# Kernel optimization log

Measured on AMD Instinct MI355X. Metric: run time of the kernel, lower is better.

The kernel has to match this reference:

```python
import jax, jax.numpy as jnp
import numpy as np

MAX_NORM = 10.0
NUM_LAYERS = 3
MARGIN = 0.1
VAE_BETA = 0.1
EPS = 1e-7
N_NODES = 100000


def logmap0(x):
    # Lorentz (k=1) log map at origin: first coord -> 0, spatial scaled
    x0 = x[..., :1]
    alpha = jnp.maximum(x0, 1.0 + EPS)
    coef = jnp.arccosh(alpha) / jnp.sqrt(jnp.maximum(alpha * alpha - 1.0, EPS))
    return jnp.concatenate([jnp.zeros_like(x0), coef * x[..., 1:]], axis=-1)


def expmap0(u, project=False):
    # Lorentz (k=1) exp map at origin; first coord of u is ignored (tangent at o)
    sp = u[..., 1:]
    n = jnp.maximum(jnp.linalg.norm(sp, axis=-1, keepdims=True), EPS)
    x_sp = jnp.sinh(n) / n * sp
    if project:
        sn = jnp.linalg.norm(x_sp, axis=-1, keepdims=True)
        x_sp = x_sp * jnp.minimum(1.0, MAX_NORM / jnp.maximum(sn, EPS))
        x0 = jnp.sqrt(1.0 + jnp.sum(x_sp * x_sp, axis=-1, keepdims=True))
    else:
        x0 = jnp.cosh(n)
    return jnp.concatenate([x0, x_sp], axis=-1)


def sqdist(x, y):
    inner = -x[..., 0] * y[..., 0] + jnp.sum(x[..., 1:] * y[..., 1:], axis=-1)
    d = jnp.arccosh(jnp.maximum(-inner, 1.0 + EPS))
    return d * d


def moe(x, W, b, gW, gb):
    gates = jax.nn.softmax(x @ gW + gb, axis=-1)              # [N,E]
    expert = jnp.einsum('nd,edo->neo', x, W) + b               # [N,E,D]
    return jnp.einsum('neo,ne->no', expert, gates)             # [N,D]


def spmm(rows, cols, vals, h):
    return jax.ops.segment_sum(vals[:, None] * h[cols], rows, num_segments=N_NODES)


def setup_inputs() -> dict:
    key = jax.random.key(0)
    ks = jax.random.split(key, 24)
    D, E, NNZ, T = 64, 8, 3200000, 262144
    Nu, Ni = 60000, 40000
    s = 0.05
    emb_user = expmap0(jax.random.normal(ks[0], (Nu, D)) * 0.1, project=True)
    emb_item = expmap0(jax.random.normal(ks[1], (Ni, D)) * 0.1, project=True)
    return {
        'emb_user': emb_user,
        'emb_item': emb_item,
        'adj_rows': jax.random.randint(ks[2], (NNZ,), 0, N_NODES, dtype=jnp.int32),
        'adj_cols': jax.random.randint(ks[3], (NNZ,), 0, N_NODES, dtype=jnp.int32),
        'adj_vals': jax.random.uniform(ks[4], (NNZ,)) * 0.05,
        'triples': jax.random.randint(ks[5], (T, 3), 0, N_NODES, dtype=jnp.int32),
        'eps': jax.random.normal(ks[6], (N_NODES, D)),
        'tW': jax.random.normal(ks[7], (E, D, D)) * s,
        'tb': jax.random.normal(ks[8], (E, D)) * s,
        'tgW': jax.random.normal(ks[9], (D, E)) * s,
        'tgb': jax.random.normal(ks[10], (E,)) * s,
        'muW': jax.random.normal(ks[11], (D, D)) * s,
        'mub': jax.random.normal(ks[12], (D,)) * s,
        'lvW': jax.random.normal(ks[13], (D, D)) * s,
        'lvb': jax.random.normal(ks[14], (D,)) * s,
        'f1W': jax.random.normal(ks[15], (D, 2 * D)) * s,
        'f1b': jax.random.normal(ks[16], (2 * D,)) * s,
        'f2W': jax.random.normal(ks[17], (2 * D, D)) * s,
        'f2b': jax.random.normal(ks[18], (D,)) * s,
        'dW': jax.random.normal(ks[19], (E, D, D)) * s,
        'db': jax.random.normal(ks[20], (E, D)) * s,
        'dgW': jax.random.normal(ks[21], (D, E)) * s,
        'dgb': jax.random.normal(ks[22], (E,)) * s,
    }


def reference(emb_user, emb_item, adj_rows, adj_cols, adj_vals, triples, eps,
              tW, tb, tgW, tgb, muW, mub, lvW, lvb,
              f1W, f1b, f2W, f2b, dW, db, dgW, dgb):
    # encode: log map frozen hyperbolic embeddings, MoE transform
    t = jnp.concatenate([logmap0(emb_user), logmap0(emb_item)], axis=0)   # [N,D]
    m = moe(t, tW, tb, tgW, tgb)                                          # [N,D]
    # VAE
    mu = m @ muW + mub
    logvar = m @ lvW + lvb
    std = jnp.exp(0.5 * logvar)
    z = expmap0(mu + eps * std, project=True)
    # hyperbolic decoder
    h = logmap0(z)
    h = jax.nn.relu(h @ f1W + f1b)
    h = h @ f2W + f2b
    h = moe(h, dW, db, dgW, dgb)
    recon = expmap0(h, project=True)
    recon_loss = jnp.mean(sqdist(recon, expmap0(m)))
    kl_loss = -0.5 * jnp.mean(1.0 + logvar - mu * mu - jnp.exp(logvar))
    # margin loss: num_layers of sparse propagation, sum of layer outputs
    res = m
    out_sum = jnp.zeros_like(m)
    for _ in range(NUM_LAYERS):
        res = spmm(adj_rows, adj_cols, adj_vals, res)
        out_sum = out_sum + res
    out = expmap0(out_sum, project=True)
    a, p, n = out[triples[:, 0]], out[triples[:, 1]], out[triples[:, 2]]
    margin_loss = jnp.sum(jax.nn.relu(sqdist(a, p) - sqdist(a, n) + MARGIN))
    return margin_loss + VAE_BETA * (recon_loss + kl_loss)
```

## Files before the change

### kernel.cpp

```cpp
#include <hip/hip_runtime.h>
#include <math.h>

#define EPSF 1e-7f
#define MAXNRM 10.0f
#define NB 782
#define RPB 128
#define EPT 16

using bf16x8 = __attribute__((ext_vector_type(8))) short;
using f32x4  = __attribute__((ext_vector_type(4))) float;
typedef unsigned short u16;

__device__ __forceinline__ float wsum(float v) {
    #pragma unroll
    for (int off = 32; off > 0; off >>= 1) v += __shfl_xor(v, off, 64);
    return v;
}

__device__ __forceinline__ u16 f2bf(float x) {
    unsigned u = __float_as_uint(x);
    unsigned r = (u + 0x7FFFu + ((u >> 16) & 1u)) >> 16;
    return (u16)r;
}
__device__ __forceinline__ float bflo(unsigned u) { return __uint_as_float(u << 16); }
__device__ __forceinline__ float bfhi(unsigned u) { return __uint_as_float(u & 0xFFFF0000u); }


__device__ __forceinline__ void body_logmap(int bid, const float* __restrict__ eu,
                                            const float* __restrict__ ei, int Nu, int Ntot,
                                            float* __restrict__ out) {
    const int lane = threadIdx.x & 63;
    const int g = lane >> 4, q = lane & 15;
    const int n = bid * 16 + (threadIdx.x >> 6) * 4 + g;
    if (n >= Ntot) return;
    const float* src = (n < Nu) ? (eu + (size_t)n * 64) : (ei + (size_t)(n - Nu) * 64);
    const float x0 = src[0];
    const float alpha = fmaxf(x0, 1.0f + EPSF);
    const float coef = acoshf(alpha) / sqrtf(fmaxf(alpha * alpha - 1.0f, EPSF));
    const float4 v = *(const float4*)(src + q * 4);
    float4 o;
    o.x = (q == 0) ? 0.0f : coef * v.x;
    o.y = coef * v.y; o.z = coef * v.z; o.w = coef * v.w;
    *(float4*)(out + ((size_t)n << 6) + q * 4) = o;
}

__device__ __forceinline__ void body_bhist(int bid, int nblk, const int* __restrict__ rows,
                                           int nnz, int* __restrict__ bhist, int* h) {
    for (int j = threadIdx.x; j < NB; j += 256) h[j] = 0;
    __syncthreads();
    for (int i = bid * 256 + threadIdx.x; i < nnz; i += nblk * 256)
        atomicAdd(&h[rows[i] >> 7], 1);
    __syncthreads();
    for (int j = threadIdx.x; j < NB; j += 256)
        if (h[j]) atomicAdd(&bhist[j], h[j]);
}

__device__ __forceinline__ void body_moe(int bid, char* smem,
    const float* __restrict__ X, float* __restrict__ Y,
    const u16* __restrict__ Wt, const u16* __restrict__ Bt,
    const float* __restrict__ GW, const float* __restrict__ GB,
    u16* __restrict__ Bhout, int Ntot)
{
    float (*sX)[68] = (float(*)[68])smem;
    float (*sG)[8]  = (float(*)[8])(smem + 17408);
    float* sGW      = (float*)(smem + 17408 + 2048);
    const int tid = threadIdx.x;
    const int n0 = bid * 64;

    for (int i = tid; i < 64 * 16; i += 256) {
        const int rr = i >> 4, cc = i & 15;
        float4 v = make_float4(0.f, 0.f, 0.f, 0.f);
        if (n0 + rr < Ntot) v = *(const float4*)(X + (size_t)(n0 + rr) * 64 + cc * 4);
        *(float4*)&sX[rr][cc * 4] = v;
    }
    for (int i = tid; i < 512; i += 256) sGW[i] = GW[i];
    __syncthreads();

    {
        const int n = tid >> 2, e0 = (tid & 3) * 2;
        float lg0 = GB[e0], lg1 = GB[e0 + 1];
        #pragma unroll 8
        for (int d = 0; d < 64; ++d) {
            const float xv = sX[n][d];
            lg0 += xv * sGW[d * 8 + e0];
            lg1 += xv * sGW[d * 8 + e0 + 1];
        }
        sG[n][e0] = lg0; sG[n][e0 + 1] = lg1;
    }
    __syncthreads();
    if (tid < 64) {
        float ex[8], mx = -1e30f, s = 0.f;
        #pragma unroll
        for (int e = 0; e < 8; ++e) mx = fmaxf(mx, sG[tid][e]);
        #pragma unroll
        for (int e = 0; e < 8; ++e) { ex[e] = expf(sG[tid][e] - mx); s += ex[e]; }
        const float inv = 1.0f / s;
        #pragma unroll
        for (int e = 0; e < 8; ++e) sG[tid][e] = ex[e] * inv;
    }
    __syncthreads();

    const int w = tid >> 6, l = tid & 63;
    const int m = l & 15, kq = l >> 4;
    const int col = w * 16 + m;

    f32x4 zero = {0.f, 0.f, 0.f, 0.f};
    f32x4 acc[4];
    #pragma unroll
    for (int rt = 0; rt < 4; ++rt) acc[rt] = zero;

    bf16x8 bcur = *(const bf16x8*)(Wt + (((size_t)col) << 6) + kq * 8);

    #pragma unroll
    for (int kk = 0; kk < 16; ++kk) {
        const int e = kk >> 1;
        const int d0 = (kk & 1) * 32 + kq * 8;
        bf16x8 bnext = bcur;
        if (kk < 15) {
            const int e2 = (kk + 1) >> 1;
            const int d02 = ((kk + 1) & 1) * 32 + kq * 8;
            bnext = *(const bf16x8*)(Wt + (((size_t)(e2 * 64 + col)) << 6) + d02);
        }
        #pragma unroll
        for (int rt = 0; rt < 4; ++rt) {
            const int row = rt * 16 + m;
            const float gme = sG[row][e];
            const float4 xa = *(const float4*)&sX[row][d0];
            const float4 xb = *(const float4*)&sX[row][d0 + 4];
            union { bf16x8 v; u16 u[8]; } af;
            af.u[0] = f2bf(gme * xa.x); af.u[1] = f2bf(gme * xa.y);
            af.u[2] = f2bf(gme * xa.z); af.u[3] = f2bf(gme * xa.w);
            af.u[4] = f2bf(gme * xb.x); af.u[5] = f2bf(gme * xb.y);
            af.u[6] = f2bf(gme * xb.z); af.u[7] = f2bf(gme * xb.w);
            acc[rt] = __builtin_amdgcn_mfma_f32_16x16x32_bf16(af.v, bcur, acc[rt], 0, 0, 0);
        }
        bcur = bnext;
    }
    {
        bf16x8 z8 = {0, 0, 0, 0, 0, 0, 0, 0};
        bf16x8 bb = z8;
        if (kq == 0) bb = *(const bf16x8*)(Bt + (col << 3));
        #pragma unroll
        for (int rt = 0; rt < 4; ++rt) {
            union { bf16x8 v; u16 u[8]; } af;
            #pragma unroll
            for (int j = 0; j < 8; ++j)
                af.u[j] = (kq == 0) ? f2bf(sG[rt * 16 + m][j]) : (u16)0;
            acc[rt] = __builtin_amdgcn_mfma_f32_16x16x32_bf16(af.v, bb, acc[rt], 0, 0, 0);
        }
    }

    #pragma unroll
    for (int rt = 0; rt < 4; ++rt) {
        #pragma unroll
        for (int r = 0; r < 4; ++r) {
            const int row = rt * 16 + kq * 4 + r;
            if (n0 + row < Ntot) {
                Y[(size_t)(n0 + row) * 64 + col] = acc[rt][r];
                if (Bhout)
                    Bhout[(((size_t)(n0 + row)) << 6) + col] = f2bf(acc[rt][r]);
            }
        }
    }
}

__device__ __forceinline__ void body_bscatter(int bid, char* smem,
    const int* __restrict__ rows, const int* __restrict__ cols,
    const float* __restrict__ vals, int nnz,
    int* __restrict__ gcur, int2* __restrict__ tmp)
{
    int* lh = (int*)smem;
    int* lb = (int*)(smem + 3128);
    const int tid = threadIdx.x;
    for (int j = tid; j < NB; j += 256) lh[j] = 0;
    __syncthreads();

    const int base = bid * (256 * EPT);
    int r[EPT], c[EPT], lp[EPT];
    float v[EPT];
    #pragma unroll
    for (int j = 0; j < EPT; ++j) {
        const int i = base + j * 256 + tid;
        if (i < nnz) {
            r[j] = rows[i]; c[j] = cols[i]; v[j] = vals[i];
            lp[j] = atomicAdd(&lh[r[j] >> 7], 1);
        }
    }
    __syncthreads();
    for (int j = tid; j < NB; j += 256)
        if (lh[j]) lb[j] = atomicAdd(&gcur[j], lh[j]);
    __syncthreads();
    #pragma unroll
    for (int j = 0; j < EPT; ++j) {
        const int i = base + j * 256 + tid;
        if (i < nnz) {
            int2 e;
            e.x = ((r[j] & 127) << 17) | c[j];
            e.y = __float_as_int(v[j]);
            tmp[lb[r[j] >> 7] + lp[j]] = e;
        }
    }
}

__device__ __forceinline__ void body_vae(int bid, char* smem,
    const float* __restrict__ M, float* __restrict__ Hout,
    const float* __restrict__ EPSN, const u16* __restrict__ WtV,
    const float* __restrict__ mub, const float* __restrict__ lvb,
    float* __restrict__ klslot, int Ntot)
{
    float (*sX)[68] = (float(*)[68])smem;
    float* sC       = (float*)(smem + 17408);
    const int tid = threadIdx.x;
    const int n0 = bid * 64;

    for (int i = tid; i < 64 * 16; i += 256) {
        const int rr = i >> 4, cc = i & 15;
        float4 v = make_float4(0.f, 0.f, 0.f, 0.f);
        if (n0 + rr < Ntot) v = *(const float4*)(M + (size_t)(n0 + rr) * 64 + cc * 4);
        *(float4*)&sX[rr][cc * 4] = v;
    }
    __syncthreads();

    const int w = tid >> 6, l = tid & 63;
    const int m = l & 15, kq = l >> 4;
    const int rowm = w * 16 + m;

    f32x4 zero = {0.f, 0.f, 0.f, 0.f};
    f32x4 acc[8];
    #pragma unroll
    for (int t = 0; t < 8; ++t) acc[t] = zero;

    #pragma unroll
    for (int ks = 0; ks < 2; ++ks) {
        const int k0 = ks * 32 + kq * 8;
        const float4 xa = *(const float4*)&sX[rowm][k0];
        const float4 xb = *(const float4*)&sX[rowm][k0 + 4];
        union { bf16x8 v; u16 u[8]; } af;
        af.u[0] = f2bf(xa.x); af.u[1] = f2bf(xa.y); af.u[2] = f2bf(xa.z); af.u[3] = f2bf(xa.w);
        af.u[4] = f2bf(xb.x); af.u[5] = f2bf(xb.y); af.u[6] = f2bf(xb.z); af.u[7] = f2bf(xb.w);
        #pragma unroll
        for (int t = 0; t < 8; ++t) {
            const bf16x8 bf = *(const bf16x8*)(WtV + (((size_t)(t * 16 + m)) << 6) + k0);
            acc[t] = __builtin_amdgcn_mfma_f32_16x16x32_bf16(af.v, bf, acc[t], 0, 0, 0);
        }
    }

    float klp = 0.f;
    float uv[4][4];
    #pragma unroll
    for (int t = 0; t < 4; ++t) {
        const int col = t * 16 + m;
        const float mb = mub[col], lb = lvb[col];
        #pragma unroll
        for (int r = 0; r < 4; ++r) {
            const int row = w * 16 + kq * 4 + r;
            const float mu = acc[t][r] + mb;
            const float lv = acc[t + 4][r] + lb;
            const float elv = expf(lv);
            float ep = 0.f;
            if (n0 + row < Ntot) {
                klp += 1.0f + lv - mu * mu - elv;
                ep = EPSN[(size_t)(n0 + row) * 64 + col];
            }
            uv[t][r] = mu + ep * expf(0.5f * lv);
        }
    }
    klp = wsum(klp);
    if (l == 0) atomicAdd(&klslot[(bid * 4 + w) & 255], klp);

    #pragma unroll
    for (int t = 0; t < 4; ++t)
        #pragma unroll
        for (int r = 0; r < 4; ++r)
            sX[w * 16 + kq * 4 + r][t * 16 + m] = uv[t][r];
    __syncthreads();

    {
        const int r2 = tid >> 2, j = tid & 3;
        float ss = 0.f;
        #pragma unroll
        for (int jj = 0; jj < 4; ++jj) {
            float4 a = *(const float4*)&sX[r2][j * 16 + jj * 4];
            if (j == 0 && jj == 0) a.x = 0.f;
            ss += a.x * a.x + a.y * a.y + a.z * a.z + a.w * a.w;
        }
        ss += __shfl_xor(ss, 1, 64);
        ss += __shfl_xor(ss, 2, 64);
        if (j == 0) {
            const float nr = fmaxf(sqrtf(ss), EPSF);
            const float r = sinhf(nr) / nr;
            const float sn = r * sqrtf(ss);
            const float scale = fminf(1.0f, MAXNRM / fmaxf(sn, EPSF));
            const float mult = r * scale;
            const float s2 = mult * mult * ss;
            const float z0 = sqrtf(1.0f + s2);
            const float alpha = fmaxf(z0, 1.0f + EPSF);
            const float coef = acoshf(alpha) / sqrtf(fmaxf(alpha * alpha - 1.0f, EPSF));
            sC[r2] = coef * mult;
        }
    }
    __syncthreads();

    for (int i = tid; i < 64 * 16; i += 256) {
        const int rr = i >> 4, cc = i & 15;
        if (n0 + rr >= Ntot) continue;
        const float4 v = *(const float4*)&sX[rr][cc * 4];
        const float sc = sC[rr];
        float4 o;
        o.x = (cc == 0) ? 0.f : sc * v.x;
        o.y = sc * v.y; o.z = sc * v.z; o.w = sc * v.w;
        *(float4*)(Hout + (size_t)(n0 + rr) * 64 + cc * 4) = o;
    }
}

__device__ __forceinline__ void body_sort(int bid, char* smem,
    const int2* __restrict__ tmp, const int* __restrict__ bstart,
    int2* __restrict__ sedge, int* __restrict__ Fout, int Ntot, int nnz)
{
    int* cnt  = (int*)smem;
    int* excl = (int*)(smem + 512);
    const int b = bid;
    const int tid = threadIdx.x;
    if (tid < RPB) cnt[tid] = 0;
    __syncthreads();
    const int s = bstart[b], t = bstart[b + 1];

    for (int i = s + tid; i < t; i += 256)
        atomicAdd(&cnt[((unsigned)tmp[i].x) >> 17], 1);
    __syncthreads();

    if (tid < 64) {
        const int a0 = cnt[2 * tid], a1 = cnt[2 * tid + 1];
        const int pairsum = a0 + a1;
        int run = pairsum;
        #pragma unroll
        for (int off = 1; off < 64; off <<= 1) {
            const int vv = __shfl_up(run, off, 64);
            if (tid >= off) run += vv;
        }
        const int ep = run - pairsum;
        excl[2 * tid] = ep;
        excl[2 * tid + 1] = ep + a0;
    }
    __syncthreads();

    const int r0 = b << 7;
    if (tid < RPB) {
        const int r = r0 + tid;
        if (r < Ntot) Fout[r] = s + excl[tid];
        cnt[tid] = excl[tid];
    }
    if (b == NB - 1 && tid == 0) Fout[Ntot] = nnz;
    __syncthreads();

    for (int i = s + tid; i < t; i += 256) {
        const int2 e = tmp[i];
        const int rib = ((unsigned)e.x) >> 17;
        const int lpos = atomicAdd(&cnt[rib], 1);
        int2 o; o.x = e.x & 0x1FFFF; o.y = e.y;
        sedge[s + lpos] = o;
    }
}


__global__ __launch_bounds__(256) void fat_prep(
    const float* tW, const float* tb, u16* Wt1, u16* Bt1,
    const float* dW, const float* db, u16* Wt2, u16* Bt2,
    const float* muW, const float* lvW, u16* WtV,
    const float* f1W, u16* Wt1f, const float* f2W, u16* Wt2f)
{
    const int b = blockIdx.x;
    if (b < 36) {
        const float* W = (b < 18) ? tW : dW;
        const float* Bb = (b < 18) ? tb : db;
        u16* Wt = (b < 18) ? Wt1 : Wt2;
        u16* Bt = (b < 18) ? Bt1 : Bt2;
        const int i = (b % 18) * 256 + threadIdx.x;
        if (i < 4096) {
            const int e = i >> 9, o = (i >> 3) & 63, dbi = i & 7;
            u16 v[8];
            #pragma unroll
            for (int j = 0; j < 8; ++j)
                v[j] = f2bf(W[((size_t)e << 12) + (size_t)(dbi * 8 + j) * 64 + o]);
            uint4 p;
            p.x = (unsigned)v[0] | ((unsigned)v[1] << 16);
            p.y = (unsigned)v[2] | ((unsigned)v[3] << 16);
            p.z = (unsigned)v[4] | ((unsigned)v[5] << 16);
            p.w = (unsigned)v[6] | ((unsigned)v[7] << 16);
            *(uint4*)(Wt + (((size_t)(e * 64 + o)) << 6) + dbi * 8) = p;
        } else if (i < 4096 + 512) {
            const int j = i - 4096, o = j >> 3, e = j & 7;
            Bt[o * 8 + e] = f2bf(Bb[e * 64 + o]);
        }
    } else if (b < 68) {
        const bool is_mu = (b < 52);
        const float* src = is_mu ? muW : lvW;
        u16* dst = is_mu ? WtV : (WtV + 4096);
        const int i = ((b - (is_mu ? 36 : 52))) * 256 + threadIdx.x;
        if (i < 4096) {
            const int o = i / 64, k = i - o * 64;
            dst[i] = f2bf(src[k * 64 + o]);
        }
    } else if (b < 100) {
        const int i = (b - 68) * 256 + threadIdx.x;
        if (i < 8192) {
            const int o = i / 64, k = i - o * 64;
            Wt1f[i] = f2bf(f1W[k * 128 + o]);
        }
    } else {
        const int i = (b - 100) * 256 + threadIdx.x;
        if (i < 8192) {
            const int o = i / 128, k = i - o * 128;
            Wt2f[i] = f2bf(f2W[k * 64 + o]);
        }
    }
}

#define NB_LOG 6250
#define NB_HIST 512
__global__ __launch_bounds__(256) void fat_log_bhist(
    const float* eu, const float* ei, int Nu, int Ntot, float* out,
    const int* rows, int nnz, int* bhist)
{
    __shared__ int h[NB];
    const int b = blockIdx.x;
    if (b < NB_LOG) {
        body_logmap(b, eu, ei, Nu, Ntot, out);
    } else {
        body_bhist(b - NB_LOG, NB_HIST, rows, nnz, bhist, h);
    }
}

#define NB_MOE 1563
__global__ __launch_bounds__(256) void fat_moe_bsc(
    const float* X, float* Y, const u16* Wt, const u16* Bt,
    const float* GW, const float* GB, u16* Bhout, int Ntot,
    const int* rows, const int* cols, const float* vals, int nnz,
    int* gcur, int2* tmp)
{
    __shared__ __align__(16) char smem[21504];
    const int b = blockIdx.x;
    if (b < NB_MOE) {
        body_moe(b, smem, X, Y, Wt, Bt, GW, GB, Bhout, Ntot);
    } else {
        body_bscatter(b - NB_MOE, smem, rows, cols, vals, nnz, gcur, tmp);
    }
}

__global__ __launch_bounds__(256) void fat_vae_sort(
    const float* M, float* Hout, const float* EPSN, const u16* WtV,
    const float* mub, const float* lvb, float* klslot, int Ntot,
    const int2* tmp, const int* bstart, int2* sedge, int* Fout, int nnz)
{
    __shared__ __align__(16) char smem[17664];
    const int b = blockIdx.x;
    if (b < NB_MOE) {
        body_vae(b, smem, M, Hout, EPSN, WtV, mub, lvb, klslot, Ntot);
    } else {
        body_sort(b - NB_MOE, smem, tmp, bstart, sedge, Fout, Ntot, nnz);
    }
}


__global__ __launch_bounds__(256) void k_moe_mfma(
    const float* __restrict__ X, float* __restrict__ Y,
    const u16* __restrict__ Wt, const u16* __restrict__ Bt,
    const float* __restrict__ GW, const float* __restrict__ GB,
    u16* __restrict__ Bhout, int Ntot)
{
    __shared__ __align__(16) char smem[21504];
    body_moe(blockIdx.x, smem, X, Y, Wt, Bt, GW, GB, Bhout, Ntot);
}

__global__ __launch_bounds__(1024) void k_bscan(const int* __restrict__ bhist,
                                                int* __restrict__ bstart, int* __restrict__ gcur) {
    __shared__ int s[1024];
    const int tid = threadIdx.x;
    int v = (tid < NB) ? bhist[tid] : 0;
    s[tid] = v;
    __syncthreads();
    for (int off = 1; off < 1024; off <<= 1) {
        int t = (tid >= off) ? s[tid - off] : 0;
        __syncthreads();
        s[tid] += t;
        __syncthreads();
    }
    if (tid < NB) {
        bstart[tid + 1] = s[tid];
        gcur[tid] = s[tid] - v;
        if (tid == 0) bstart[0] = 0;
    }
}

__global__ __launch_bounds__(256) void k_ffn_mfma(
    float* __restrict__ Hio,
    const u16* __restrict__ Wt1f, const float* __restrict__ f1b,
    const u16* __restrict__ Wt2f, const float* __restrict__ f2b, int Ntot)
{
    __shared__ float sH[64][68];
    __shared__ u16 sH1[64][136];
    const int tid = threadIdx.x;
    const int n0 = blockIdx.x * 64;

    for (int i = tid; i < 64 * 16; i += 256) {
        const int rr = i >> 4, cc = i & 15;
        float4 v = make_float4(0.f, 0.f, 0.f, 0.f);
        if (n0 + rr < Ntot) v = *(const float4*)(Hio + (size_t)(n0 + rr) * 64 + cc * 4);
        *(float4*)&sH[rr][cc * 4] = v;
    }
    __syncthreads();

    const int w = tid >> 6, l = tid & 63;
    const int m = l & 15, kq = l >> 4;
    const int rowm = w * 16 + m;

    f32x4 zero = {0.f, 0.f, 0.f, 0.f};
    f32x4 acc1[8];
    #pragma unroll
    for (int t = 0; t < 8; ++t) acc1[t] = zero;

    #pragma unroll
    for (int ks = 0; ks < 2; ++ks) {
        const int k0 = ks * 32 + kq * 8;
        const float4 xa = *(const float4*)&sH[rowm][k0];
        const float4 xb = *(const float4*)&sH[rowm][k0 + 4];
        union { bf16x8 v; u16 u[8]; } af;
        af.u[0] = f2bf(xa.x); af.u[1] = f2bf(xa.y); af.u[2] = f2bf(xa.z); af.u[3] = f2bf(xa.w);
        af.u[4] = f2bf(xb.x); af.u[5] = f2bf(xb.y); af.u[6] = f2bf(xb.z); af.u[7] = f2bf(xb.w);
        #pragma unroll
        for (int t = 0; t < 8; ++t) {
            const bf16x8 bf = *(const bf16x8*)(Wt1f + (((size_t)(t * 16 + m)) << 6) + k0);
            acc1[t] = __builtin_amdgcn_mfma_f32_16x16x32_bf16(af.v, bf, acc1[t], 0, 0, 0);
        }
    }
    #pragma unroll
    for (int t = 0; t < 8; ++t) {
        const float bb = f1b[t * 16 + m];
        #pragma unroll
        for (int r = 0; r < 4; ++r)
            sH1[w * 16 + kq * 4 + r][t * 16 + m] = f2bf(fmaxf(acc1[t][r] + bb, 0.f));
    }
    __syncthreads();

    f32x4 acc2[4];
    #pragma unroll
    for (int t = 0; t < 4; ++t) acc2[t] = zero;
    #pragma unroll
    for (int ks = 0; ks < 4; ++ks) {
        const int k0 = ks * 32 + kq * 8;
        const bf16x8 af = *(const bf16x8*)&sH1[rowm][k0];
        #pragma unroll
        for (int t = 0; t < 4; ++t) {
            const bf16x8 bf = *(const bf16x8*)(Wt2f + (((size_t)(t * 16 + m)) << 7) + k0);
            acc2[t] = __builtin_amdgcn_mfma_f32_16x16x32_bf16(af, bf, acc2[t], 0, 0, 0);
        }
    }
    #pragma unroll
    for (int t = 0; t < 4; ++t) {
        const float bb = f2b[t * 16 + m];
        #pragma unroll
        for (int r = 0; r < 4; ++r) {
            const int row = w * 16 + kq * 4 + r;
            if (n0 + row < Ntot)
                Hio[(size_t)(n0 + row) * 64 + t * 16 + m] = acc2[t][r] + bb;
        }
    }
}

__global__ __launch_bounds__(256) void k_recon(
    const float* __restrict__ HM, const float* __restrict__ M,
    int Ntot, float* __restrict__ slot)
{
    const int lane = threadIdx.x & 63;
    const int g = lane >> 4, q = lane & 15;
    const int n = blockIdx.x * 16 + (threadIdx.x >> 6) * 4 + g;

    float ssh = 0.f, ssm = 0.f, dot = 0.f;
    if (n < Ntot) {
        const float4 h = *(const float4*)(HM + ((size_t)n << 6) + q * 4);
        const float4 m = *(const float4*)(M  + ((size_t)n << 6) + q * 4);
        const float hx = (q == 0) ? 0.f : h.x;
        const float mx = (q == 0) ? 0.f : m.x;
        ssh = hx * hx + h.y * h.y + h.z * h.z + h.w * h.w;
        ssm = mx * mx + m.y * m.y + m.z * m.z + m.w * m.w;
        dot = hx * mx + h.y * m.y + h.z * m.z + h.w * m.w;
    }
    #pragma unroll
    for (int off = 1; off < 16; off <<= 1) {
        ssh += __shfl_xor(ssh, off, 64);
        ssm += __shfl_xor(ssm, off, 64);
        dot += __shfl_xor(dot, off, 64);
    }

    float part = 0.f;
    if (q == 0 && n < Ntot) {
        const float nm = fmaxf(sqrtf(ssm), EPSF);
        const float em0 = coshf(nm);
        const float rm = sinhf(nm) / nm;

        const float nh = fmaxf(sqrtf(ssh), EPSF);
        const float rh = sinhf(nh) / nh;
        const float sn = rh * sqrtf(ssh);
        const float scale = fminf(1.0f, MAXNRM / fmaxf(sn, EPSF));
        const float mult = rh * scale;
        const float rec0 = sqrtf(1.0f + mult * mult * ssh);

        const float inner = mult * rm * dot - rec0 * em0;
        const float dd = acoshf(fmaxf(-inner, 1.0f + EPSF));
        part = dd * dd;
    }
    part = wsum(part);
    __shared__ float sb[4];
    if (lane == 0) sb[threadIdx.x >> 6] = part;
    __syncthreads();
    if (threadIdx.x == 0)
        atomicAdd(&slot[blockIdx.x & 255], sb[0] + sb[1] + sb[2] + sb[3]);
}

__global__ __launch_bounds__(256) void k_spmm(
    const u16* __restrict__ in, u16* __restrict__ outb,
    const int* __restrict__ F, const int2* __restrict__ sedge, int Ntot, int nnz)
{
    const int r = blockIdx.x * 4 + (threadIdx.x >> 6);
    if (r >= Ntot) return;
    const int lane = threadIdx.x & 63;
    const int g = lane >> 3, q = lane & 7;
    const int e0 = F[r], e1 = F[r + 1];
    const int nnzm1 = nnz - 1;

    float acc0[8], acc1[8];
    #pragma unroll
    for (int j = 0; j < 8; ++j) { acc0[j] = 0.f; acc1[j] = 0.f; }

    int2 edA, edB;
    uint4 hbA, hbB;
    {
        const int ea = e0 + g, eb = e0 + 8 + g;
        edA = sedge[min(ea, nnzm1)]; if (ea >= e1) edA.y = 0;
        edB = sedge[min(eb, nnzm1)]; if (eb >= e1) edB.y = 0;
        hbA = *(const uint4*)(in + (((size_t)edA.x) << 6) + q * 8);
        hbB = *(const uint4*)(in + (((size_t)edB.x) << 6) + q * 8);
    }

    for (int base = e0; base < e1; base += 16) {
        const int na = base + 16 + g, nb = base + 24 + g;
        int2 edA2 = sedge[min(na, nnzm1)]; if (na >= e1) edA2.y = 0;
        int2 edB2 = sedge[min(nb, nnzm1)]; if (nb >= e1) edB2.y = 0;
        const uint4 hbA2 = *(const uint4*)(in + (((size_t)edA2.x) << 6) + q * 8);
        const uint4 hbB2 = *(const uint4*)(in + (((size_t)edB2.x) << 6) + q * 8);

        {
            const float v = __int_as_float(edA.y);
            acc0[0] += v * bflo(hbA.x);
            acc0[1] += v * bfhi(hbA.x);
            acc0[2] += v * bflo(hbA.y);
            acc0[3] += v * bfhi(hbA.y);
            acc0[4] += v * bflo(hbA.z);
            acc0[5] += v * bfhi(hbA.z);
            acc0[6] += v * bflo(hbA.w);
            acc0[7] += v * bfhi(hbA.w);
        }
        {
            const float v = __int_as_float(edB.y);
            acc1[0] += v * bflo(hbB.x);
            acc1[1] += v * bfhi(hbB.x);
            acc1[2] += v * bflo(hbB.y);
            acc1[3] += v * bfhi(hbB.y);
            acc1[4] += v * bflo(hbB.z);
            acc1[5] += v * bfhi(hbB.z);
            acc1[6] += v * bflo(hbB.w);
            acc1[7] += v * bfhi(hbB.w);
        }
        edA = edA2; edB = edB2; hbA = hbA2; hbB = hbB2;
    }
    float a0[8];
    #pragma unroll
    for (int j = 0; j < 8; ++j) a0[j] = acc0[j] + acc1[j];

    #pragma unroll
    for (int off = 8; off < 64; off <<= 1)
        #pragma unroll
        for (int j = 0; j < 8; ++j) a0[j] += __shfl_xor(a0[j], off, 64);

    if (g == 0) {
        const size_t ob = (((size_t)r) << 6) + q * 8;
        uint4 p;
        p.x = (unsigned)f2bf(a0[0]) | ((unsigned)f2bf(a0[1]) << 16);
        p.y = (unsigned)f2bf(a0[2]) | ((unsigned)f2bf(a0[3]) << 16);
        p.z = (unsigned)f2bf(a0[4]) | ((unsigned)f2bf(a0[5]) << 16);
        p.w = (unsigned)f2bf(a0[6]) | ((unsigned)f2bf(a0[7]) << 16);
        *(uint4*)(outb + ob) = p;
    }
}

__global__ __launch_bounds__(256) void k_osum(
    const u16* __restrict__ r1, const u16* __restrict__ r2,
    const u16* __restrict__ r3, u16* __restrict__ outb, int Ntot)
{
    const int lane = threadIdx.x & 63;
    const int g = lane >> 4, q = lane & 15;
    const int n = blockIdx.x * 16 + (threadIdx.x >> 6) * 4 + g;
    if (n >= Ntot) return;
    const size_t ob = ((size_t)n << 6) + q * 4;
    const uint2 a = *(const uint2*)(r1 + ob);
    const uint2 b = *(const uint2*)(r2 + ob);
    const uint2 c = *(const uint2*)(r3 + ob);
    float s0 = bflo(a.x) + bflo(b.x) + bflo(c.x);
    float s1 = bfhi(a.x) + bfhi(b.x) + bfhi(c.x);
    float s2 = bflo(a.y) + bflo(b.y) + bflo(c.y);
    float s3 = bfhi(a.y) + bfhi(b.y) + bfhi(c.y);
    const float v0 = (q == 0) ? 0.f : s0;
    float ss = v0 * v0 + s1 * s1 + s2 * s2 + s3 * s3;
    #pragma unroll
    for (int off = 1; off < 16; off <<= 1) ss += __shfl_xor(ss, off, 64);
    const float nr = fmaxf(sqrtf(ss), EPSF);
    const float r = sinhf(nr) / nr;
    const float sn = r * sqrtf(ss);
    const float scale = fminf(1.0f, MAXNRM / fmaxf(sn, EPSF));
    const float mult = r * scale;
    const float o0 = (q == 0) ? sqrtf(1.0f + mult * mult * ss) : mult * s0;
    uint2 p;
    p.x = (unsigned)f2bf(o0) | ((unsigned)f2bf(mult * s1) << 16);
    p.y = (unsigned)f2bf(mult * s2) | ((unsigned)f2bf(mult * s3) << 16);
    *(uint2*)(outb + ob) = p;
}

__global__ __launch_bounds__(256) void k_triples(
    const u16* __restrict__ Ob, const int* __restrict__ tri,
    int T, float* __restrict__ slot)
{
    const int lane = threadIdx.x & 63;
    const int g = lane >> 4, q = lane & 15;
    const int wid = blockIdx.x * 4 + (threadIdx.x >> 6);
    const int stride = gridDim.x * 4 * 4;

    float racc = 0.f;
    int t = wid * 4 + g;

    uint2 ca, cp, cn;
    if (t < T) {
        const int a = tri[3 * t], p = tri[3 * t + 1], nn = tri[3 * t + 2];
        ca = *(const uint2*)(Ob + (((size_t)a) << 6) + q * 4);
        cp = *(const uint2*)(Ob + (((size_t)p) << 6) + q * 4);
        cn = *(const uint2*)(Ob + (((size_t)nn) << 6) + q * 4);
    }

    for (; t < T; ) {
        const int tn = t + stride;
        const int tc = min(tn, T - 1);
        const int a2 = tri[3 * tc], p2 = tri[3 * tc + 1], n2 = tri[3 * tc + 2];
        const uint2 na_ = *(const uint2*)(Ob + (((size_t)a2) << 6) + q * 4);
        const uint2 np_ = *(const uint2*)(Ob + (((size_t)p2) << 6) + q * 4);
        const uint2 nn_ = *(const uint2*)(Ob + (((size_t)n2) << 6) + q * 4);

        {
            const float a0 = bflo(ca.x), a1 = bfhi(ca.x), a2f = bflo(ca.y), a3 = bfhi(ca.y);
            const float p0 = bflo(cp.x), p1 = bfhi(cp.x), p2f = bflo(cp.y), p3 = bfhi(cp.y);
            const float n0 = bflo(cn.x), n1 = bfhi(cn.x), n2f = bflo(cn.y), n3 = bfhi(cn.y);
            const float s0 = (q == 0) ? -1.f : 1.f;
            float i1 = s0 * a0 * p0 + a1 * p1 + a2f * p2f + a3 * p3;
            float i2 = s0 * a0 * n0 + a1 * n1 + a2f * n2f + a3 * n3;
            #pragma unroll
            for (int off = 1; off < 16; off <<= 1) {
                i1 += __shfl_xor(i1, off, 64);
                i2 += __shfl_xor(i2, off, 64);
            }
            if (q == 0) {
                const float d1 = acoshf(fmaxf(-i1, 1.0f + EPSF));
                const float d2 = acoshf(fmaxf(-i2, 1.0f + EPSF));
                const float l = d1 * d1 - d2 * d2 + 0.1f;
                if (l > 0.f) racc += l;
            }
        }
        ca = na_; cp = np_; cn = nn_;
        t = tn;
    }

    racc = wsum(racc);
    __shared__ float sb[4];
    if (lane == 0) sb[threadIdx.x >> 6] = racc;
    __syncthreads();
    if (threadIdx.x == 0)
        atomicAdd(&slot[blockIdx.x & 255], sb[0] + sb[1] + sb[2] + sb[3]);
}

__global__ void k_final(const float* __restrict__ slots, float* __restrict__ out, int Ntot)
{
    const int tid = threadIdx.x;
    float m = slots[tid], r = slots[256 + tid], k = slots[512 + tid];
    m = wsum(m); r = wsum(r); k = wsum(k);
    __shared__ float sm[4], sr[4], sk[4];
    if ((tid & 63) == 0) { sm[tid >> 6] = m; sr[tid >> 6] = r; sk[tid >> 6] = k; }
    __syncthreads();
    if (tid == 0) {
        const float M = sm[0] + sm[1] + sm[2] + sm[3];
        const float R = sr[0] + sr[1] + sr[2] + sr[3];
        const float K = sk[0] + sk[1] + sk[2] + sk[3];
        const float recon = R / (float)Ntot;
        const float kl = -0.5f * K / ((float)Ntot * 64.0f);
        out[0] = M + 0.1f * (recon + kl);
    }
}

extern "C" void kernel_launch(void* const* d_in, const int* in_sizes, int n_in,
                              void* d_out, int out_size, void* d_ws, size_t ws_size,
                              hipStream_t stream)
{
    const float* emb_user = (const float*)d_in[0];
    const float* emb_item = (const float*)d_in[1];
    const int*   adj_rows = (const int*)d_in[2];
    const int*   adj_cols = (const int*)d_in[3];
    const float* adj_vals = (const float*)d_in[4];
    const int*   triples  = (const int*)d_in[5];
    const float* epsin    = (const float*)d_in[6];
    const float* tW  = (const float*)d_in[7];
    const float* tb  = (const float*)d_in[8];
    const float* tgW = (const float*)d_in[9];
    const float* tgb = (const float*)d_in[10];
    const float* muW = (const float*)d_in[11];
    const float* mub = (const float*)d_in[12];
    const float* lvW = (const float*)d_in[13];
    const float* lvb = (const float*)d_in[14];
    const float* f1W = (const float*)d_in[15];
    const float* f1b = (const float*)d_in[16];
    const float* f2W = (const float*)d_in[17];
    const float* f2b = (const float*)d_in[18];
    const float* dW  = (const float*)d_in[19];
    const float* db  = (const float*)d_in[20];
    const float* dgW = (const float*)d_in[21];
    const float* dgb = (const float*)d_in[22];

    const int Nu = in_sizes[0] / 64, Ni = in_sizes[1] / 64;
    const int N = Nu + Ni;
    const int NNZ = in_sizes[4];
    const int T = in_sizes[5] / 3;

    float* ws = (float*)d_ws;
    size_t off = 0;
    float* slots = ws + off; off += 1024;
    float* A  = ws + off; off += (size_t)N * 64;
    float* B  = ws + off; off += (size_t)N * 64;
    float* C  = ws + off; off += (size_t)N * 64;
    float* D  = ws + off; off += (size_t)N * 64;
    float* E  = ws + off; off += (size_t)N * 64;
    int*   F  = (int*)(ws + off); off += (size_t)N + 64;
    int*   bstart = (int*)(ws + off); off += 1024;
    int*   bhist  = (int*)(ws + off); off += 1024;
    int*   gcur   = (int*)(ws + off); off += 1024;
    u16* Wt1 = (u16*)(ws + off); off += 16384;
    u16* Bt1 = (u16*)(ws + off); off += 256;
    u16* Wt2 = (u16*)(ws + off); off += 16384;
    u16* Bt2 = (u16*)(ws + off); off += 256;
    u16* WtV  = (u16*)(ws + off); off += 4096;
    u16* Wt1f = (u16*)(ws + off); off += 4096;
    u16* Wt2f = (u16*)(ws + off); off += 4096;

    int2* tmp   = (int2*)C;
    int2* sedge = (int2*)D;
    u16* Bh  = (u16*)E;
    u16* Hb1 = (u16*)E + (size_t)N * 64;
    u16* Hb2 = (u16*)C;
    u16* Hb3 = (u16*)A;
    u16* Ob  = (u16*)B;

    hipMemsetAsync(slots, 0, 1024 * sizeof(float), stream);
    hipMemsetAsync(bhist, 0, 1024 * sizeof(int), stream);

    const int nb16 = (N + 15) / 16;
    const int nb64 = (N + 63) / 64;
    const int ns1 = (NNZ + 256 * EPT - 1) / (256 * EPT);

    fat_prep<<<132, 256, 0, stream>>>(tW, tb, Wt1, Bt1, dW, db, Wt2, Bt2,
                                      muW, lvW, WtV, f1W, Wt1f, f2W, Wt2f);

    fat_log_bhist<<<NB_LOG + NB_HIST, 256, 0, stream>>>(emb_user, emb_item, Nu, N, A,
                                                        adj_rows, NNZ, bhist);

    k_bscan<<<1, 1024, 0, stream>>>(bhist, bstart, gcur);

    fat_moe_bsc<<<NB_MOE + 782, 256, 0, stream>>>(A, B, Wt1, Bt1, tgW, tgb, Bh, N,
                                                  adj_rows, adj_cols, adj_vals, NNZ, gcur, tmp);

    fat_vae_sort<<<NB_MOE + NB, 256, 0, stream>>>(B, A, epsin, WtV, mub, lvb, slots + 512, N,
                                                  tmp, bstart, sedge, F, NNZ);

    k_ffn_mfma<<<nb64, 256, 0, stream>>>(A, Wt1f, f1b, Wt2f, f2b, N);
    k_moe_mfma<<<nb64, 256, 0, stream>>>(A, C, Wt2, Bt2, dgW, dgb, nullptr, N);
    k_recon<<<nb16, 256, 0, stream>>>(C, B, N, slots + 256);

    k_spmm<<<(N + 3) / 4, 256, 0, stream>>>(Bh,  Hb1, F, sedge, N, NNZ);
    k_spmm<<<(N + 3) / 4, 256, 0, stream>>>(Hb1, Hb2, F, sedge, N, NNZ);
    k_spmm<<<(N + 3) / 4, 256, 0, stream>>>(Hb2, Hb3, F, sedge, N, NNZ);

    k_osum<<<nb16, 256, 0, stream>>>(Hb1, Hb2, Hb3, Ob, N);

    k_triples<<<2048, 256, 0, stream>>>(Ob, triples, T, slots);
    k_final<<<1, 256, 0, stream>>>(slots, (float*)d_out, N);
}
```

Baseline: 459.7 us.

## Co-schedule decoder FFN, MoE and recon blocks with the three SpMM passes

Merges the decoder stages (FFN, second MoE, recon loss) with the three independent sparse propagation passes into three combined kernels, dispatching blocks by index to either the dense body or the SpMM body. The aim is to run compute-bound MFMA work alongside the memory-bound gathers and to remove separate launches. The second SpMM output now reuses the buffer that held the first SpMM's input, because C is written concurrently by the MoE. In exchange, SpMM blocks now carry the larger shared-memory allocation of the combined kernels, which may reduce their occupancy.

```diff
diff --git a/kernel.cpp b/kernel.cpp
--- a/kernel.cpp
+++ b/kernel.cpp
@@ -359,6 +359,208 @@
         const int lpos = atomicAdd(&cnt[rib], 1);
         int2 o; o.x = e.x & 0x1FFFF; o.y = e.y;
         sedge[s + lpos] = o;
+    }
+}
+
+__device__ __forceinline__ void body_ffn(int bid, char* smem,
+    float* __restrict__ Hio,
+    const u16* __restrict__ Wt1f, const float* __restrict__ f1b,
+    const u16* __restrict__ Wt2f, const float* __restrict__ f2b, int Ntot)
+{
+    float (*sH)[68] = (float(*)[68])smem;
+    u16 (*sH1)[136] = (u16(*)[136])smem;
+    const int tid = threadIdx.x;
+    const int n0 = bid * 64;
+
+    for (int i = tid; i < 64 * 16; i += 256) {
+        const int rr = i >> 4, cc = i & 15;
+        float4 v = make_float4(0.f, 0.f, 0.f, 0.f);
+        if (n0 + rr < Ntot) v = *(const float4*)(Hio + (size_t)(n0 + rr) * 64 + cc * 4);
+        *(float4*)&sH[rr][cc * 4] = v;
+    }
+    __syncthreads();
+
+    const int w = tid >> 6, l = tid & 63;
+    const int m = l & 15, kq = l >> 4;
+    const int rowm = w * 16 + m;
+
+    f32x4 zero = {0.f, 0.f, 0.f, 0.f};
+    f32x4 acc1[8];
+    #pragma unroll
+    for (int t = 0; t < 8; ++t) acc1[t] = zero;
+
+    #pragma unroll
+    for (int ks = 0; ks < 2; ++ks) {
+        const int k0 = ks * 32 + kq * 8;
+        const float4 xa = *(const float4*)&sH[rowm][k0];
+        const float4 xb = *(const float4*)&sH[rowm][k0 + 4];
+        union { bf16x8 v; u16 u[8]; } af;
+        af.u[0] = f2bf(xa.x); af.u[1] = f2bf(xa.y); af.u[2] = f2bf(xa.z); af.u[3] = f2bf(xa.w);
+        af.u[4] = f2bf(xb.x); af.u[5] = f2bf(xb.y); af.u[6] = f2bf(xb.z); af.u[7] = f2bf(xb.w);
+        #pragma unroll
+        for (int t = 0; t < 8; ++t) {
+            const bf16x8 bf = *(const bf16x8*)(Wt1f + (((size_t)(t * 16 + m)) << 6) + k0);
+            acc1[t] = __builtin_amdgcn_mfma_f32_16x16x32_bf16(af.v, bf, acc1[t], 0, 0, 0);
+        }
+    }
+    __syncthreads();
+    #pragma unroll
+    for (int t = 0; t < 8; ++t) {
+        const float bb = f1b[t * 16 + m];
+        #pragma unroll
+        for (int r = 0; r < 4; ++r)
+            sH1[w * 16 + kq * 4 + r][t * 16 + m] = f2bf(fmaxf(acc1[t][r] + bb, 0.f));
+    }
+    __syncthreads();
+
+    f32x4 acc2[4];
+    #pragma unroll
+    for (int t = 0; t < 4; ++t) acc2[t] = zero;
+    #pragma unroll
+    for (int ks = 0; ks < 4; ++ks) {
+        const int k0 = ks * 32 + kq * 8;
+        const bf16x8 af = *(const bf16x8*)&sH1[rowm][k0];
+        #pragma unroll
+        for (int t = 0; t < 4; ++t) {
+            const bf16x8 bf = *(const bf16x8*)(Wt2f + (((size_t)(t * 16 + m)) << 7) + k0);
+            acc2[t] = __builtin_amdgcn_mfma_f32_16x16x32_bf16(af, bf, acc2[t], 0, 0, 0);
+        }
+    }
+    #pragma unroll
+    for (int t = 0; t < 4; ++t) {
+        const float bb = f2b[t * 16 + m];
+        #pragma unroll
+        for (int r = 0; r < 4; ++r) {
+            const int row = w * 16 + kq * 4 + r;
+            if (n0 + row < Ntot)
+                Hio[(size_t)(n0 + row) * 64 + t * 16 + m] = acc2[t][r] + bb;
+        }
+    }
+}
+
+__device__ __forceinline__ void body_recon(int bid, char* smem,
+    const float* __restrict__ HM, const float* __restrict__ M,
+    int Ntot, float* __restrict__ slot)
+{
+    float* sb = (float*)smem;
+    const int lane = threadIdx.x & 63;
+    const int g = lane >> 4, q = lane & 15;
+    const int n = bid * 16 + (threadIdx.x >> 6) * 4 + g;
+
+    float ssh = 0.f, ssm = 0.f, dot = 0.f;
+    if (n < Ntot) {
+        const float4 h = *(const float4*)(HM + ((size_t)n << 6) + q * 4);
+        const float4 m = *(const float4*)(M  + ((size_t)n << 6) + q * 4);
+        const float hx = (q == 0) ? 0.f : h.x;
+        const float mx = (q == 0) ? 0.f : m.x;
+        ssh = hx * hx + h.y * h.y + h.z * h.z + h.w * h.w;
+        ssm = mx * mx + m.y * m.y + m.z * m.z + m.w * m.w;
+        dot = hx * mx + h.y * m.y + h.z * m.z + h.w * m.w;
+    }
+    #pragma unroll
+    for (int off = 1; off < 16; off <<= 1) {
+        ssh += __shfl_xor(ssh, off, 64);
+        ssm += __shfl_xor(ssm, off, 64);
+        dot += __shfl_xor(dot, off, 64);
+    }
+
+    float part = 0.f;
+    if (q == 0 && n < Ntot) {
+        const float nm = fmaxf(sqrtf(ssm), EPSF);
+        const float em0 = coshf(nm);
+        const float rm = sinhf(nm) / nm;
+
+        const float nh = fmaxf(sqrtf(ssh), EPSF);
+        const float rh = sinhf(nh) / nh;
+        const float sn = rh * sqrtf(ssh);
+        const float scale = fminf(1.0f, MAXNRM / fmaxf(sn, EPSF));
+        const float mult = rh * scale;
+        const float rec0 = sqrtf(1.0f + mult * mult * ssh);
+
+        const float inner = mult * rm * dot - rec0 * em0;
+        const float dd = acoshf(fmaxf(-inner, 1.0f + EPSF));
+        part = dd * dd;
+    }
+    part = wsum(part);
+    if (lane == 0) sb[threadIdx.x >> 6] = part;
+    __syncthreads();
+    if (threadIdx.x == 0)
+        atomicAdd(&slot[bid & 255], sb[0] + sb[1] + sb[2] + sb[3]);
+}
+
+__device__ __forceinline__ void body_spmm(int bid,
+    const u16* __restrict__ in, u16* __restrict__ outb,
+    const int* __restrict__ F, const int2* __restrict__ sedge, int Ntot, int nnz)
+{
+    const int r = bid * 4 + (threadIdx.x >> 6);
+    if (r >= Ntot) return;
+    const int lane = threadIdx.x & 63;
+    const int g = lane >> 3, q = lane & 7;
+    const int e0 = F[r], e1 = F[r + 1];
+    const int nnzm1 = nnz - 1;
+
+    float acc0[8], acc1[8];
+    #pragma unroll
+    for (int j = 0; j < 8; ++j) { acc0[j] = 0.f; acc1[j] = 0.f; }
+
+    int2 edA, edB;
+    uint4 hbA, hbB;
+    {
+        const int ea = e0 + g, eb = e0 + 8 + g;
+        edA = sedge[min(ea, nnzm1)]; if (ea >= e1) edA.y = 0;
+        edB = sedge[min(eb, nnzm1)]; if (eb >= e1) edB.y = 0;
+        hbA = *(const uint4*)(in + (((size_t)edA.x) << 6) + q * 8);
+        hbB = *(const uint4*)(in + (((size_t)edB.x) << 6) + q * 8);
+    }
+
+    for (int base = e0; base < e1; base += 16) {
+        const int na = base + 16 + g, nb = base + 24 + g;
+        int2 edA2 = sedge[min(na, nnzm1)]; if (na >= e1) edA2.y = 0;
+        int2 edB2 = sedge[min(nb, nnzm1)]; if (nb >= e1) edB2.y = 0;
+        const uint4 hbA2 = *(const uint4*)(in + (((size_t)edA2.x) << 6) + q * 8);
+        const uint4 hbB2 = *(const uint4*)(in + (((size_t)edB2.x) << 6) + q * 8);
+
+        {
+            const float v = __int_as_float(edA.y);
+            acc0[0] += v * bflo(hbA.x);
+            acc0[1] += v * bfhi(hbA.x);
+            acc0[2] += v * bflo(hbA.y);
+            acc0[3] += v * bfhi(hbA.y);
+            acc0[4] += v * bflo(hbA.z);
+            acc0[5] += v * bfhi(hbA.z);
+            acc0[6] += v * bflo(hbA.w);
+            acc0[7] += v * bfhi(hbA.w);
+        }
+        {
+            const float v = __int_as_float(edB.y);
+            acc1[0] += v * bflo(hbB.x);
+            acc1[1] += v * bfhi(hbB.x);
+            acc1[2] += v * bflo(hbB.y);
+            acc1[3] += v * bfhi(hbB.y);
+            acc1[4] += v * bflo(hbB.z);
+            acc1[5] += v * bfhi(hbB.z);
+            acc1[6] += v * bflo(hbB.w);
+            acc1[7] += v * bfhi(hbB.w);
+        }
+        edA = edA2; edB = edB2; hbA = hbA2; hbB = hbB2;
+    }
+    float a0[8];
+    #pragma unroll
+    for (int j = 0; j < 8; ++j) a0[j] = acc0[j] + acc1[j];
+
+    #pragma unroll
+    for (int off = 8; off < 64; off <<= 1)
+        #pragma unroll
+        for (int j = 0; j < 8; ++j) a0[j] += __shfl_xor(a0[j], off, 64);
+
+    if (g == 0) {
+        const size_t ob = (((size_t)r) << 6) + q * 8;
+        uint4 p;
+        p.x = (unsigned)f2bf(a0[0]) | ((unsigned)f2bf(a0[1]) << 16);
+        p.y = (unsigned)f2bf(a0[2]) | ((unsigned)f2bf(a0[3]) << 16);
+        p.z = (unsigned)f2bf(a0[4]) | ((unsigned)f2bf(a0[5]) << 16);
+        p.w = (unsigned)f2bf(a0[6]) | ((unsigned)f2bf(a0[7]) << 16);
+        *(uint4*)(outb + ob) = p;
     }
 }
 
@@ -461,16 +663,48 @@
     }
 }
 
-
-__global__ __launch_bounds__(256) void k_moe_mfma(
-    const float* __restrict__ X, float* __restrict__ Y,
-    const u16* __restrict__ Wt, const u16* __restrict__ Bt,
-    const float* __restrict__ GW, const float* __restrict__ GB,
-    u16* __restrict__ Bhout, int Ntot)
+#define NB_SPMM 25000
+__global__ __launch_bounds__(256) void fat_ffn_spmm(
+    float* Hio, const u16* Wt1f, const float* f1b,
+    const u16* Wt2f, const float* f2b, int Ntot,
+    const u16* in, u16* outb, const int* F, const int2* sedge, int nnz)
+{
+    __shared__ __align__(16) char smem[17408];
+    const int b = blockIdx.x;
+    if (b < NB_MOE) {
+        body_ffn(b, smem, Hio, Wt1f, f1b, Wt2f, f2b, Ntot);
+    } else {
+        body_spmm(b - NB_MOE, in, outb, F, sedge, Ntot, nnz);
+    }
+}
+
+__global__ __launch_bounds__(256) void fat_moe2_spmm(
+    const float* X, float* Y, const u16* Wt, const u16* Bt,
+    const float* GW, const float* GB, int Ntot,
+    const u16* in, u16* outb, const int* F, const int2* sedge, int nnz)
 {
     __shared__ __align__(16) char smem[21504];
-    body_moe(blockIdx.x, smem, X, Y, Wt, Bt, GW, GB, Bhout, Ntot);
-}
+    const int b = blockIdx.x;
+    if (b < NB_MOE) {
+        body_moe(b, smem, X, Y, Wt, Bt, GW, GB, (u16*)0, Ntot);
+    } else {
+        body_spmm(b - NB_MOE, in, outb, F, sedge, Ntot, nnz);
+    }
+}
+
+__global__ __launch_bounds__(256) void fat_recon_spmm(
+    const float* HM, const float* M, int Ntot, float* slot,
+    const u16* in, u16* outb, const int* F, const int2* sedge, int nnz)
+{
+    __shared__ __align__(16) char smem[64];
+    const int b = blockIdx.x;
+    if (b < NB_LOG) {
+        body_recon(b, smem, HM, M, Ntot, slot);
+    } else {
+        body_spmm(b - NB_LOG, in, outb, F, sedge, Ntot, nnz);
+    }
+}
+
 
 __global__ __launch_bounds__(1024) void k_bscan(const int* __restrict__ bhist,
                                                 int* __restrict__ bstart, int* __restrict__ gcur) {
@@ -489,207 +723,6 @@
         bstart[tid + 1] = s[tid];
         gcur[tid] = s[tid] - v;
         if (tid == 0) bstart[0] = 0;
-    }
-}
-
-__global__ __launch_bounds__(256) void k_ffn_mfma(
-    float* __restrict__ Hio,
-    const u16* __restrict__ Wt1f, const float* __restrict__ f1b,
-    const u16* __restrict__ Wt2f, const float* __restrict__ f2b, int Ntot)
-{
-    __shared__ float sH[64][68];
-    __shared__ u16 sH1[64][136];
-    const int tid = threadIdx.x;
-    const int n0 = blockIdx.x * 64;
-
-    for (int i = tid; i < 64 * 16; i += 256) {
-        const int rr = i >> 4, cc = i & 15;
-        float4 v = make_float4(0.f, 0.f, 0.f, 0.f);
-        if (n0 + rr < Ntot) v = *(const float4*)(Hio + (size_t)(n0 + rr) * 64 + cc * 4);
-        *(float4*)&sH[rr][cc * 4] = v;
-    }
-    __syncthreads();
-
-    const int w = tid >> 6, l = tid & 63;
-    const int m = l & 15, kq = l >> 4;
-    const int rowm = w * 16 + m;
-
-    f32x4 zero = {0.f, 0.f, 0.f, 0.f};
-    f32x4 acc1[8];
-    #pragma unroll
-    for (int t = 0; t < 8; ++t) acc1[t] = zero;
-
-    #pragma unroll
-    for (int ks = 0; ks < 2; ++ks) {
-        const int k0 = ks * 32 + kq * 8;
-        const float4 xa = *(const float4*)&sH[rowm][k0];
-        const float4 xb = *(const float4*)&sH[rowm][k0 + 4];
-        union { bf16x8 v; u16 u[8]; } af;
-        af.u[0] = f2bf(xa.x); af.u[1] = f2bf(xa.y); af.u[2] = f2bf(xa.z); af.u[3] = f2bf(xa.w);
-        af.u[4] = f2bf(xb.x); af.u[5] = f2bf(xb.y); af.u[6] = f2bf(xb.z); af.u[7] = f2bf(xb.w);
-        #pragma unroll
-        for (int t = 0; t < 8; ++t) {
-            const bf16x8 bf = *(const bf16x8*)(Wt1f + (((size_t)(t * 16 + m)) << 6) + k0);
-            acc1[t] = __builtin_amdgcn_mfma_f32_16x16x32_bf16(af.v, bf, acc1[t], 0, 0, 0);
-        }
-    }
-    #pragma unroll
-    for (int t = 0; t < 8; ++t) {
-        const float bb = f1b[t * 16 + m];
-        #pragma unroll
-        for (int r = 0; r < 4; ++r)
-            sH1[w * 16 + kq * 4 + r][t * 16 + m] = f2bf(fmaxf(acc1[t][r] + bb, 0.f));
-    }
-    __syncthreads();
-
-    f32x4 acc2[4];
-    #pragma unroll
-    for (int t = 0; t < 4; ++t) acc2[t] = zero;
-    #pragma unroll
-    for (int ks = 0; ks < 4; ++ks) {
-        const int k0 = ks * 32 + kq * 8;
-        const bf16x8 af = *(const bf16x8*)&sH1[rowm][k0];
-        #pragma unroll
-        for (int t = 0; t < 4; ++t) {
-            const bf16x8 bf = *(const bf16x8*)(Wt2f + (((size_t)(t * 16 + m)) << 7) + k0);
-            acc2[t] = __builtin_amdgcn_mfma_f32_16x16x32_bf16(af, bf, acc2[t], 0, 0, 0);
-        }
-    }
-    #pragma unroll
-    for (int t = 0; t < 4; ++t) {
-        const float bb = f2b[t * 16 + m];
-        #pragma unroll
-        for (int r = 0; r < 4; ++r) {
-            const int row = w * 16 + kq * 4 + r;
-            if (n0 + row < Ntot)
-                Hio[(size_t)(n0 + row) * 64 + t * 16 + m] = acc2[t][r] + bb;
-        }
-    }
-}
-
-__global__ __launch_bounds__(256) void k_recon(
-    const float* __restrict__ HM, const float* __restrict__ M,
-    int Ntot, float* __restrict__ slot)
-{
-    const int lane = threadIdx.x & 63;
-    const int g = lane >> 4, q = lane & 15;
-    const int n = blockIdx.x * 16 + (threadIdx.x >> 6) * 4 + g;
-
-    float ssh = 0.f, ssm = 0.f, dot = 0.f;
-    if (n < Ntot) {
-        const float4 h = *(const float4*)(HM + ((size_t)n << 6) + q * 4);
-        const float4 m = *(const float4*)(M  + ((size_t)n << 6) + q * 4);
-        const float hx = (q == 0) ? 0.f : h.x;
-        const float mx = (q == 0) ? 0.f : m.x;
-        ssh = hx * hx + h.y * h.y + h.z * h.z + h.w * h.w;
-        ssm = mx * mx + m.y * m.y + m.z * m.z + m.w * m.w;
-        dot = hx * mx + h.y * m.y + h.z * m.z + h.w * m.w;
-    }
-    #pragma unroll
-    for (int off = 1; off < 16; off <<= 1) {
-        ssh += __shfl_xor(ssh, off, 64);
-        ssm += __shfl_xor(ssm, off, 64);
-        dot += __shfl_xor(dot, off, 64);
-    }
-
-    float part = 0.f;
-    if (q == 0 && n < Ntot) {
-        const float nm = fmaxf(sqrtf(ssm), EPSF);
-        const float em0 = coshf(nm);
-        const float rm = sinhf(nm) / nm;
-
-        const float nh = fmaxf(sqrtf(ssh), EPSF);
-        const float rh = sinhf(nh) / nh;
-        const float sn = rh * sqrtf(ssh);
-        const float scale = fminf(1.0f, MAXNRM / fmaxf(sn, EPSF));
-        const float mult = rh * scale;
-        const float rec0 = sqrtf(1.0f + mult * mult * ssh);
-
-        const float inner = mult * rm * dot - rec0 * em0;
-        const float dd = acoshf(fmaxf(-inner, 1.0f + EPSF));
-        part = dd * dd;
-    }
-    part = wsum(part);
-    __shared__ float sb[4];
-    if (lane == 0) sb[threadIdx.x >> 6] = part;
-    __syncthreads();
-    if (threadIdx.x == 0)
-        atomicAdd(&slot[blockIdx.x & 255], sb[0] + sb[1] + sb[2] + sb[3]);
-}
-
-__global__ __launch_bounds__(256) void k_spmm(
-    const u16* __restrict__ in, u16* __restrict__ outb,
-    const int* __restrict__ F, const int2* __restrict__ sedge, int Ntot, int nnz)
-{
-    const int r = blockIdx.x * 4 + (threadIdx.x >> 6);
-    if (r >= Ntot) return;
-    const int lane = threadIdx.x & 63;
-    const int g = lane >> 3, q = lane & 7;
-    const int e0 = F[r], e1 = F[r + 1];
-    const int nnzm1 = nnz - 1;
-
-    float acc0[8], acc1[8];
-    #pragma unroll
-    for (int j = 0; j < 8; ++j) { acc0[j] = 0.f; acc1[j] = 0.f; }
-
-    int2 edA, edB;
-    uint4 hbA, hbB;
-    {
-        const int ea = e0 + g, eb = e0 + 8 + g;
-        edA = sedge[min(ea, nnzm1)]; if (ea >= e1) edA.y = 0;
-        edB = sedge[min(eb, nnzm1)]; if (eb >= e1) edB.y = 0;
-        hbA = *(const uint4*)(in + (((size_t)edA.x) << 6) + q * 8);
-        hbB = *(const uint4*)(in + (((size_t)edB.x) << 6) + q * 8);
-    }
-
-    for (int base = e0; base < e1; base += 16) {
-        const int na = base + 16 + g, nb = base + 24 + g;
-        int2 edA2 = sedge[min(na, nnzm1)]; if (na >= e1) edA2.y = 0;
-        int2 edB2 = sedge[min(nb, nnzm1)]; if (nb >= e1) edB2.y = 0;
-        const uint4 hbA2 = *(const uint4*)(in + (((size_t)edA2.x) << 6) + q * 8);
-        const uint4 hbB2 = *(const uint4*)(in + (((size_t)edB2.x) << 6) + q * 8);
-
-        {
-            const float v = __int_as_float(edA.y);
-            acc0[0] += v * bflo(hbA.x);
-            acc0[1] += v * bfhi(hbA.x);
-            acc0[2] += v * bflo(hbA.y);
-            acc0[3] += v * bfhi(hbA.y);
-            acc0[4] += v * bflo(hbA.z);
-            acc0[5] += v * bfhi(hbA.z);
-            acc0[6] += v * bflo(hbA.w);
-            acc0[7] += v * bfhi(hbA.w);
-        }
-        {
-            const float v = __int_as_float(edB.y);
-            acc1[0] += v * bflo(hbB.x);
-            acc1[1] += v * bfhi(hbB.x);
-            acc1[2] += v * bflo(hbB.y);
-            acc1[3] += v * bfhi(hbB.y);
-            acc1[4] += v * bflo(hbB.z);
-            acc1[5] += v * bfhi(hbB.z);
-            acc1[6] += v * bflo(hbB.w);
-            acc1[7] += v * bfhi(hbB.w);
-        }
-        edA = edA2; edB = edB2; hbA = hbA2; hbB = hbB2;
-    }
-    float a0[8];
-    #pragma unroll
-    for (int j = 0; j < 8; ++j) a0[j] = acc0[j] + acc1[j];
-
-    #pragma unroll
-    for (int off = 8; off < 64; off <<= 1)
-        #pragma unroll
-        for (int j = 0; j < 8; ++j) a0[j] += __shfl_xor(a0[j], off, 64);
-
-    if (g == 0) {
-        const size_t ob = (((size_t)r) << 6) + q * 8;
-        uint4 p;
-        p.x = (unsigned)f2bf(a0[0]) | ((unsigned)f2bf(a0[1]) << 16);
-        p.y = (unsigned)f2bf(a0[2]) | ((unsigned)f2bf(a0[3]) << 16);
-        p.z = (unsigned)f2bf(a0[4]) | ((unsigned)f2bf(a0[5]) << 16);
-        p.w = (unsigned)f2bf(a0[6]) | ((unsigned)f2bf(a0[7]) << 16);
-        *(uint4*)(outb + ob) = p;
     }
 }
 
@@ -859,7 +892,7 @@
     int2* sedge = (int2*)D;
     u16* Bh  = (u16*)E;
     u16* Hb1 = (u16*)E + (size_t)N * 64;
-    u16* Hb2 = (u16*)C;
+    u16* Hb2 = (u16*)E;
     u16* Hb3 = (u16*)A;
     u16* Ob  = (u16*)B;
 
@@ -867,8 +900,6 @@
     hipMemsetAsync(bhist, 0, 1024 * sizeof(int), stream);
 
     const int nb16 = (N + 15) / 16;
-    const int nb64 = (N + 63) / 64;
-    const int ns1 = (NNZ + 256 * EPT - 1) / (256 * EPT);
 
     fat_prep<<<132, 256, 0, stream>>>(tW, tb, Wt1, Bt1, dW, db, Wt2, Bt2,
                                       muW, lvW, WtV, f1W, Wt1f, f2W, Wt2f);
@@ -884,13 +915,14 @@
     fat_vae_sort<<<NB_MOE + NB, 256, 0, stream>>>(B, A, epsin, WtV, mub, lvb, slots + 512, N,
                                                   tmp, bstart, sedge, F, NNZ);
 
-    k_ffn_mfma<<<nb64, 256, 0, stream>>>(A, Wt1f, f1b, Wt2f, f2b, N);
-    k_moe_mfma<<<nb64, 256, 0, stream>>>(A, C, Wt2, Bt2, dgW, dgb, nullptr, N);
-    k_recon<<<nb16, 256, 0, stream>>>(C, B, N, slots + 256);
-
-    k_spmm<<<(N + 3) / 4, 256, 0, stream>>>(Bh,  Hb1, F, sedge, N, NNZ);
-    k_spmm<<<(N + 3) / 4, 256, 0, stream>>>(Hb1, Hb2, F, sedge, N, NNZ);
-    k_spmm<<<(N + 3) / 4, 256, 0, stream>>>(Hb2, Hb3, F, sedge, N, NNZ);
+    fat_ffn_spmm<<<NB_MOE + NB_SPMM, 256, 0, stream>>>(A, Wt1f, f1b, Wt2f, f2b, N,
+                                                       Bh, Hb1, F, sedge, NNZ);
+
+    fat_moe2_spmm<<<NB_MOE + NB_SPMM, 256, 0, stream>>>(A, C, Wt2, Bt2, dgW, dgb, N,
+                                                        Hb1, Hb2, F, sedge, NNZ);
+
+    fat_recon_spmm<<<NB_LOG + NB_SPMM, 256, 0, stream>>>(C, B, N, slots + 256,
+                                                         Hb2, Hb3, F, sedge, NNZ);
 
     k_osum<<<nb16, 256, 0, stream>>>(Hb1, Hb2, Hb3, Ob, N);
 
```

Measured after the change: 503.4 us. 1.09x slower.
